# Kernel tuning notes

Measured on AMD Instinct MI355X. Metric: run time of the kernel, lower is better.

## Reference

```python
import jax, jax.numpy as jnp
import numpy as np

N_SPACE = 197  # spatial tokens (ViT-B/16: 196 patches + CLS)
T = 8          # frames, fixed by space_time_pos shape (197*8, dim)
H = 12         # heads


def setup_inputs() -> dict:
    key = jax.random.key(0)
    ks = jax.random.split(key, 8)
    dim = 768
    B = 8
    Nq = 1576
    scale = dim ** -0.5
    return {
        "s_x": jax.random.normal(ks[0], (N_SPACE, B * T, dim), jnp.float32),
        "t_x": jax.random.normal(ks[1], (B, Nq, dim), jnp.float32),
        "space_time_pos": scale * jax.random.normal(ks[2], (N_SPACE * T, dim), jnp.float32),
        "q_w": jax.random.normal(ks[3], (dim, dim), jnp.float32) * 0.02,
        "q_b": jnp.zeros((dim,), jnp.float32),
        "kv_w": jax.random.normal(ks[4], (2 * dim, dim), jnp.float32) * 0.02,
        "kv_b": jnp.zeros((2 * dim,), jnp.float32),
        "proj_w": jax.random.normal(ks[5], (dim, dim), jnp.float32) * 0.02,
        "proj_b": jnp.zeros((dim,), jnp.float32),
    }


def reference(s_x, t_x, space_time_pos, q_w, q_b, kv_w, kv_b, proj_w, proj_b):
    n, BT, dim = s_x.shape
    B, Nq, _ = t_x.shape
    t = BT // B
    head_dim = dim // H
    scale = head_dim ** -0.5

    # rearrange 'n (b t) d -> b (t n) d'
    s = s_x.reshape(n, B, t, dim).transpose(1, 2, 0, 3).reshape(B, t * n, dim)
    s = s + space_time_pos  # (B, t*n, dim)

    # Q from t_x, K/V from s
    q = t_x @ q_w.T + q_b                      # (B, Nq, dim)
    kv = s @ kv_w.T + kv_b                     # (B, t*n, 2*dim)
    Nk = t * n
    # 'b n (e h d) -> e b h n d'
    kv = kv.reshape(B, Nk, 2, H, head_dim).transpose(2, 0, 3, 1, 4)
    k, v = kv[0], kv[1]                        # (B, H, Nk, hd)
    q = q.reshape(B, Nq, H, head_dim).transpose(0, 2, 1, 3) * scale  # (B, H, Nq, hd)

    attn = jnp.einsum('bhqd,bhkd->bhqk', q, k)
    attn = jax.nn.softmax(attn, axis=-1)
    out = jnp.einsum('bhqk,bhkd->bhqd', attn, v)   # (B, H, Nq, hd)
    out = out.transpose(0, 2, 1, 3).reshape(B, Nq, dim)
    return out @ proj_w.T + proj_b
```

## Files before the change

kernel.cpp:

```cpp
#include <hip/hip_runtime.h>
#include <stdint.h>

#define NSPACE 197
#define TFRAMES 8
#define NH 12
#define DIM 768
#define HD 64
#define BATCH 8
#define NQ 1576
#define NK 1576
#define M_REAL 12608
#define M_PAD 12672
#define VT_LD 1600

typedef __attribute__((ext_vector_type(8))) short s16x8;
typedef __attribute__((ext_vector_type(4))) short s16x4;
typedef __attribute__((ext_vector_type(4))) float f32x4;

__device__ inline uint16_t f2bf(float f) {
    union { float f; uint32_t i; } c; c.f = f;
    uint32_t r = c.i + 0x7FFF + ((c.i >> 16) & 1);
    return (uint16_t)(r >> 16);
}

__device__ inline uint32_t cvtpk_bf16(float lo, float hi) {
    uint32_t r;
    asm("v_cvt_pk_bf16_f32 %0, %1, %2" : "=v"(r) : "v"(lo), "v"(hi));
    return r;
}

__device__ inline float exp2_raw(float x) { return __builtin_amdgcn_exp2f(x); }

__device__ inline void gld_lds16(const uint16_t* g, uint16_t* l) {
    __builtin_amdgcn_global_load_lds(
        (const __attribute__((address_space(1))) void*)g,
        (__attribute__((address_space(3))) void*)l,
        16, 0, 0);
}


__global__ void conv_f2b(const float* __restrict__ src, uint16_t* __restrict__ dst, int n8) {
    int chunk = blockIdx.x * 256 + threadIdx.x;
    if (chunk >= n8) return;
    size_t off = (size_t)chunk * 8;
    float4 a = *(const float4*)(src + off);
    float4 b = *(const float4*)(src + off + 4);
    union { s16x8 v; uint32_t u[4]; } o;
    o.u[0] = cvtpk_bf16(a.x, a.y);
    o.u[1] = cvtpk_bf16(a.z, a.w);
    o.u[2] = cvtpk_bf16(b.x, b.y);
    o.u[3] = cvtpk_bf16(b.z, b.w);
    *(s16x8*)(dst + off) = o.v;
}

__global__ void fill_x(const float* __restrict__ t_x, uint16_t* __restrict__ x_pad) {
    int chunk = blockIdx.x * 256 + threadIdx.x;
    const int total = M_PAD * (DIM / 8);
    if (chunk >= total) return;
    size_t off = (size_t)chunk * 8;
    s16x8 o;
    if (off < (size_t)M_REAL * DIM) {
        float4 a = *(const float4*)(t_x + off);
        float4 b = *(const float4*)(t_x + off + 4);
        union { s16x8 v; uint32_t u[4]; } p;
        p.u[0] = cvtpk_bf16(a.x, a.y);
        p.u[1] = cvtpk_bf16(a.z, a.w);
        p.u[2] = cvtpk_bf16(b.x, b.y);
        p.u[3] = cvtpk_bf16(b.z, b.w);
        o = p.v;
    } else {
        for (int j = 0; j < 8; j++) o[j] = 0;
    }
    *(s16x8*)(x_pad + off) = o;
}

__global__ void fill_s(const float* __restrict__ s_x, const float* __restrict__ pos,
                       uint16_t* __restrict__ s_pad) {
    int chunk = blockIdx.x * 256 + threadIdx.x;
    const int total = M_PAD * (DIM / 8);
    if (chunk >= total) return;
    int i = chunk / (DIM / 8);
    int cc = chunk - i * (DIM / 8);
    int d0 = cc * 8;
    uint16_t* dst = s_pad + (size_t)i * DIM + d0;
    if (i >= M_REAL) {
        s16x8 z; for (int j = 0; j < 8; j++) z[j] = 0;
        *(s16x8*)dst = z;
        return;
    }
    int b = i / NK, rr = i - b * NK;
    int t_i = rr / NSPACE, n_i = rr - t_i * NSPACE;
    const float* src = s_x + ((size_t)(n_i * (BATCH * TFRAMES) + b * TFRAMES + t_i)) * DIM + d0;
    const float* ps = pos + (size_t)rr * DIM + d0;
    float4 a0 = *(const float4*)src;
    float4 a1 = *(const float4*)(src + 4);
    float4 p0 = *(const float4*)ps;
    float4 p1 = *(const float4*)(ps + 4);
    union { s16x8 v; uint32_t u[4]; } o;
    o.u[0] = cvtpk_bf16(a0.x + p0.x, a0.y + p0.y);
    o.u[1] = cvtpk_bf16(a0.z + p0.z, a0.w + p0.w);
    o.u[2] = cvtpk_bf16(a1.x + p1.x, a1.y + p1.y);
    o.u[3] = cvtpk_bf16(a1.z + p1.z, a1.w + p1.w);
    *(s16x8*)dst = o.v;
}

template <int MODE>
__global__ __launch_bounds__(256)
void gemm_bt(const uint16_t* __restrict__ A, const uint16_t* __restrict__ W,
             const float* __restrict__ bias,
             uint16_t* __restrict__ out0, uint16_t* __restrict__ out1,
             float* __restrict__ outf) {
    __shared__ uint16_t As[2][128 * 32];
    __shared__ uint16_t Bs[2][128 * 32];
    const int t = threadIdx.x;
    const int lane = t & 63, w = t >> 6;
    const int r16 = lane & 15, quad = lane >> 4;
    const int wm = w >> 1, wn = w & 1;
    const int m0 = blockIdx.y * 128;
    const int n0 = blockIdx.x * 128;

    const int srow = w * 32 + (lane >> 2);
    const int scol = (lane & 3) * 8;
    const uint16_t* Ag = A + (size_t)(m0 + srow) * DIM + scol;
    const uint16_t* Wg = W + (size_t)(n0 + srow) * DIM + scol;
    const int lbase = w * 32 * 32;

    f32x4 acc[4][4];
    for (int a = 0; a < 4; a++)
        for (int bb = 0; bb < 4; bb++)
            for (int r = 0; r < 4; r++) acc[a][bb][r] = 0.f;

    auto stage = [&](int kkoff, int buf) {
        gld_lds16(Ag + kkoff, &As[buf][lbase]);
        gld_lds16(Ag + kkoff + (size_t)16 * DIM, &As[buf][lbase + 16 * 32]);
        gld_lds16(Wg + kkoff, &Bs[buf][lbase]);
        gld_lds16(Wg + kkoff + (size_t)16 * DIM, &Bs[buf][lbase + 16 * 32]);
    };
    auto compute = [&](int buf) {
        s16x8 af[4], bfr[4];
        #pragma unroll
        for (int mt = 0; mt < 4; mt++)
            af[mt] = *(const s16x8*)&As[buf][(wm * 64 + mt * 16 + r16) * 32 + quad * 8];
        #pragma unroll
        for (int nt = 0; nt < 4; nt++)
            bfr[nt] = *(const s16x8*)&Bs[buf][(wn * 64 + nt * 16 + r16) * 32 + quad * 8];
        #pragma unroll
        for (int mt = 0; mt < 4; mt++)
            #pragma unroll
            for (int nt = 0; nt < 4; nt++)
                acc[mt][nt] = __builtin_amdgcn_mfma_f32_16x16x32_bf16(af[mt], bfr[nt], acc[mt][nt], 0, 0, 0);
    };

    stage(0, 0);
    __syncthreads();

    for (int kk = 0; kk < DIM; kk += 64) {
        stage(kk + 32, 1);
        compute(0);
        __syncthreads();
        if (kk + 64 < DIM) stage(kk + 64, 0);
        compute(1);
        __syncthreads();
    }

    for (int mt = 0; mt < 4; mt++)
        for (int nt = 0; nt < 4; nt++) {
            int col = n0 + wn * 64 + nt * 16 + r16;
            float bz = bias[col];
            int rowb = m0 + wm * 64 + mt * 16 + quad * 4;
            for (int r = 0; r < 4; r++) {
                int i = rowb + r;
                if (i >= M_REAL) continue;
                float v = acc[mt][nt][r] + bz;
                if (MODE == 0) {
                    int b = i / NQ, nq = i - b * NQ;
                    int h = col >> 6, d = col & 63;
                    out0[(size_t)(((b * NH + h) * NQ) + nq) * HD + d] = f2bf(v * 0.18033688011112042f);
                } else if (MODE == 1) {
                    int b = i / NK, nk = i - b * NK;
                    if (col < DIM) {
                        int h = col >> 6, d = col & 63;
                        out0[(size_t)(((b * NH + h) * NK) + nk) * HD + d] = f2bf(v);
                    } else {
                        int c2 = col - DIM;
                        int h = c2 >> 6, d = c2 & 63;
                        out1[(size_t)(((b * NH + h) * NK) + nk) * HD + d] = f2bf(v);
                    }
                } else {
                    outf[(size_t)i * DIM + col] = v;
                }
            }
        }
}

__global__ __launch_bounds__(256)
void transpose_v(const uint16_t* __restrict__ v, uint16_t* __restrict__ vt) {
    __shared__ uint16_t T[64 * 72];
    int tile = blockIdx.x, bh = blockIdx.y;
    int nk0 = tile * 64;
    const uint16_t* V = v + (size_t)bh * NK * HD;
    uint16_t* VT = vt + (size_t)bh * HD * VT_LD;
    int tid = threadIdx.x;
    int rr = tid >> 3;
    int c8 = (tid & 7) * 8;
    for (int p = 0; p < 2; p++) {
        int lr = p * 32 + rr;
        int nk = nk0 + lr;
        s16x8 val;
        if (nk < NK) val = *(const s16x8*)(V + (size_t)nk * HD + c8);
        else for (int j = 0; j < 8; j++) val[j] = 0;
        for (int j = 0; j < 8; j++)
            T[(c8 + j) * 72 + lr] = (uint16_t)val[j];
    }
    __syncthreads();
    for (int p = 0; p < 2; p++) {
        int d = p * 32 + rr;
        s16x8 o = *(const s16x8*)&T[d * 72 + c8];
        *(s16x8*)(VT + (size_t)d * VT_LD + nk0 + c8) = o;
    }
}

#define NITER 50
__global__ __launch_bounds__(256)
void flash_attn(const uint16_t* __restrict__ q_buf, const uint16_t* __restrict__ k_buf,
                const uint16_t* __restrict__ vt_buf, uint16_t* __restrict__ ao) {
    __shared__ uint16_t Kb[2][32 * 72];
    __shared__ uint16_t Vb[2][64 * 40];
    int h = blockIdx.y, b = blockIdx.z;
    int tid = threadIdx.x;
    int lane = tid & 63, w = tid >> 6;
    int r16 = lane & 15, quad = lane >> 4;
    size_t bh = (size_t)(b * NH + h);
    const uint16_t* Q = q_buf + bh * NQ * HD;
    const uint16_t* K = k_buf + bh * NK * HD;
    const uint16_t* VT = vt_buf + bh * HD * VT_LD;
    int q0 = blockIdx.x * 128 + w * 32;

    const int kg = tid >> 3;
    const int kc = (tid & 7) * 8;
    const int kslot = ((kg >> 3) << 2) + (kg & 3) + ((kg & 4) ? 16 : 0);
    const int vd = tid >> 2;
    const int vc = (tid & 3) * 8;
    const uint16_t* Kg = K + (size_t)kg * HD + kc;
    const uint16_t* Vg = VT + (size_t)vd * VT_LD + vc;
    uint16_t* Kw = &Kb[0][kslot * 72 + kc];
    uint16_t* Vw = &Vb[0][vd * 40 + vc];
    const int KBSZ = 32 * 72, VBSZ = 64 * 40;

    s16x8 qf[2][2];
    for (int m = 0; m < 2; m++) {
        int qrow = q0 + m * 16 + r16;
        if (qrow < NQ) {
            qf[m][0] = *(const s16x8*)(Q + (size_t)qrow * HD + quad * 8);
            qf[m][1] = *(const s16x8*)(Q + (size_t)qrow * HD + 32 + quad * 8);
        } else {
            for (int j = 0; j < 8; j++) { qf[m][0][j] = 0; qf[m][1][j] = 0; }
        }
    }

    f32x4 z4;
    for (int r = 0; r < 4; r++) z4[r] = 0.f;

    f32x4 oT[2][4];
    f32x4 lsum4[2];
    for (int m = 0; m < 2; m++) {
        for (int dt = 0; dt < 4; dt++)
            for (int r = 0; r < 4; r++) oT[m][dt][r] = 0.f;
        for (int r = 0; r < 4; r++) lsum4[m][r] = 0.f;
    }

    {
        s16x8 kv = *(const s16x8*)Kg;
        s16x8 vv = *(const s16x8*)Vg;
        *(s16x8*)Kw = kv;
        *(s16x8*)Vw = vv;
    }
    __syncthreads();

    for (int it = 0; it < NITER - 1; it++) {
        int kb = it * 32;
        int cur = it & 1, nxt = cur ^ 1;
        s16x8 knv = *(const s16x8*)(Kg + (size_t)(kb + 32) * HD);
        s16x8 vnv = *(const s16x8*)(Vg + kb + 32);

        const uint16_t* Kc = &Kb[cur][0];
        const uint16_t* Vc = &Vb[cur][0];
        s16x8 kfA0 = *(const s16x8*)(Kc + r16 * 72 + quad * 8);
        s16x8 kfA1 = *(const s16x8*)(Kc + r16 * 72 + 32 + quad * 8);
        s16x8 kfB0 = *(const s16x8*)(Kc + (16 + r16) * 72 + quad * 8);
        s16x8 kfB1 = *(const s16x8*)(Kc + (16 + r16) * 72 + 32 + quad * 8);

        s16x8 pf[2];
        #pragma unroll
        for (int m = 0; m < 2; m++) {
            f32x4 sA = __builtin_amdgcn_mfma_f32_16x16x32_bf16(kfA0, qf[m][0], z4, 0, 0, 0);
            sA = __builtin_amdgcn_mfma_f32_16x16x32_bf16(kfA1, qf[m][1], sA, 0, 0, 0);
            f32x4 sB = __builtin_amdgcn_mfma_f32_16x16x32_bf16(kfB0, qf[m][0], z4, 0, 0, 0);
            sB = __builtin_amdgcn_mfma_f32_16x16x32_bf16(kfB1, qf[m][1], sB, 0, 0, 0);
            f32x4 pA, pB;
            #pragma unroll
            for (int r = 0; r < 4; r++) { pA[r] = exp2_raw(sA[r]); pB[r] = exp2_raw(sB[r]); }
            lsum4[m] += pA;
            lsum4[m] += pB;
            union { s16x8 v; uint32_t u[4]; } pk;
            pk.u[0] = cvtpk_bf16(pA[0], pA[1]);
            pk.u[1] = cvtpk_bf16(pA[2], pA[3]);
            pk.u[2] = cvtpk_bf16(pB[0], pB[1]);
            pk.u[3] = cvtpk_bf16(pB[2], pB[3]);
            pf[m] = pk.v;
        }
        #pragma unroll
        for (int dt = 0; dt < 4; dt++) {
            s16x8 vf = *(const s16x8*)(Vc + (dt * 16 + r16) * 40 + quad * 8);
            oT[0][dt] = __builtin_amdgcn_mfma_f32_16x16x32_bf16(vf, pf[0], oT[0][dt], 0, 0, 0);
            oT[1][dt] = __builtin_amdgcn_mfma_f32_16x16x32_bf16(vf, pf[1], oT[1][dt], 0, 0, 0);
        }
        *(s16x8*)(Kw + nxt * KBSZ) = knv;
        *(s16x8*)(Vw + nxt * VBSZ) = vnv;
        __syncthreads();
    }

    {
        const int it = NITER - 1;
        const int kb = it * 32;
        const int cur = it & 1;
        const uint16_t* Kc = &Kb[cur][0];
        const uint16_t* Vc = &Vb[cur][0];
        s16x8 kfA0 = *(const s16x8*)(Kc + r16 * 72 + quad * 8);
        s16x8 kfA1 = *(const s16x8*)(Kc + r16 * 72 + 32 + quad * 8);
        s16x8 kfB0 = *(const s16x8*)(Kc + (16 + r16) * 72 + quad * 8);
        s16x8 kfB1 = *(const s16x8*)(Kc + (16 + r16) * 72 + 32 + quad * 8);

        s16x8 pf[2];
        #pragma unroll
        for (int m = 0; m < 2; m++) {
            f32x4 sA = __builtin_amdgcn_mfma_f32_16x16x32_bf16(kfA0, qf[m][0], z4, 0, 0, 0);
            sA = __builtin_amdgcn_mfma_f32_16x16x32_bf16(kfA1, qf[m][1], sA, 0, 0, 0);
            f32x4 sB = __builtin_amdgcn_mfma_f32_16x16x32_bf16(kfB0, qf[m][0], z4, 0, 0, 0);
            sB = __builtin_amdgcn_mfma_f32_16x16x32_bf16(kfB1, qf[m][1], sB, 0, 0, 0);
            f32x4 pA, pB;
            #pragma unroll
            for (int r = 0; r < 4; r++) {
                pA[r] = (kb + quad * 8 + r < NK)     ? exp2_raw(sA[r]) : 0.f;
                pB[r] = (kb + quad * 8 + 4 + r < NK) ? exp2_raw(sB[r]) : 0.f;
            }
            lsum4[m] += pA;
            lsum4[m] += pB;
            union { s16x8 v; uint32_t u[4]; } pk;
            pk.u[0] = cvtpk_bf16(pA[0], pA[1]);
            pk.u[1] = cvtpk_bf16(pA[2], pA[3]);
            pk.u[2] = cvtpk_bf16(pB[0], pB[1]);
            pk.u[3] = cvtpk_bf16(pB[2], pB[3]);
            pf[m] = pk.v;
        }
        #pragma unroll
        for (int dt = 0; dt < 4; dt++) {
            s16x8 vf = *(const s16x8*)(Vc + (dt * 16 + r16) * 40 + quad * 8);
            oT[0][dt] = __builtin_amdgcn_mfma_f32_16x16x32_bf16(vf, pf[0], oT[0][dt], 0, 0, 0);
            oT[1][dt] = __builtin_amdgcn_mfma_f32_16x16x32_bf16(vf, pf[1], oT[1][dt], 0, 0, 0);
        }
    }

    #pragma unroll
    for (int m = 0; m < 2; m++) {
        float rs = lsum4[m][0] + lsum4[m][1] + lsum4[m][2] + lsum4[m][3];
        rs += __shfl_xor(rs, 16);
        rs += __shfl_xor(rs, 32);
        int q = q0 + m * 16 + r16;
        if (q >= NQ) continue;
        float inv = 1.0f / rs;
        size_t rowoff = (size_t)(b * NQ + q) * DIM + h * HD;
        #pragma unroll
        for (int dt = 0; dt < 4; dt++) {
            union { s16x4 v; uint32_t u[2]; } o;
            o.u[0] = cvtpk_bf16(oT[m][dt][0] * inv, oT[m][dt][1] * inv);
            o.u[1] = cvtpk_bf16(oT[m][dt][2] * inv, oT[m][dt][3] * inv);
            *(s16x4*)(ao + rowoff + dt * 16 + quad * 4) = o.v;
        }
    }
}

extern "C" void kernel_launch(void* const* d_in, const int* in_sizes, int n_in,
                              void* d_out, int out_size, void* d_ws, size_t ws_size,
                              hipStream_t stream) {
    const float* s_x    = (const float*)d_in[0];
    const float* t_x    = (const float*)d_in[1];
    const float* pos    = (const float*)d_in[2];
    const float* q_w    = (const float*)d_in[3];
    const float* q_b    = (const float*)d_in[4];
    const float* kv_w   = (const float*)d_in[5];
    const float* kv_b   = (const float*)d_in[6];
    const float* proj_w = (const float*)d_in[7];
    const float* proj_b = (const float*)d_in[8];
    float* out = (float*)d_out;

    char* ws = (char*)d_ws;
    size_t off = 0;
    auto carve = [&](size_t bytes) {
        void* p = ws + off;
        off += (bytes + 255) & ~(size_t)255;
        return p;
    };
    uint16_t* x_pad  = (uint16_t*)carve((size_t)M_PAD * DIM * 2);
    uint16_t* s_pad  = (uint16_t*)carve((size_t)M_PAD * DIM * 2);
    uint16_t* q_buf  = (uint16_t*)carve((size_t)BATCH * NH * NQ * HD * 2);
    uint16_t* k_buf  = (uint16_t*)carve((size_t)BATCH * NH * NK * HD * 2);
    uint16_t* vt_buf = (uint16_t*)carve((size_t)BATCH * NH * HD * VT_LD * 2);
    uint16_t* wbuf   = (uint16_t*)carve((size_t)2 * DIM * DIM * 2);
    if (off > ws_size) return;
    uint16_t* v_buf = x_pad;
    uint16_t* ao    = x_pad;

    const int fill_blocks = (M_PAD * (DIM / 8) + 255) / 256;
    const int wq8 = DIM * DIM / 8, wkv8 = 2 * DIM * DIM / 8;

    fill_x<<<fill_blocks, 256, 0, stream>>>(t_x, x_pad);
    fill_s<<<fill_blocks, 256, 0, stream>>>(s_x, pos, s_pad);

    conv_f2b<<<(wq8 + 255) / 256, 256, 0, stream>>>(q_w, wbuf, wq8);
    gemm_bt<0><<<dim3(DIM / 128, M_PAD / 128), 256, 0, stream>>>(x_pad, wbuf, q_b, q_buf, nullptr, nullptr);

    conv_f2b<<<(wkv8 + 255) / 256, 256, 0, stream>>>(kv_w, wbuf, wkv8);
    gemm_bt<1><<<dim3(2 * DIM / 128, M_PAD / 128), 256, 0, stream>>>(s_pad, wbuf, kv_b, k_buf, v_buf, nullptr);
    transpose_v<<<dim3(VT_LD / 64, BATCH * NH), 256, 0, stream>>>(v_buf, vt_buf);

    flash_attn<<<dim3((NQ + 127) / 128, NH, BATCH), 256, 0, stream>>>(q_buf, k_buf, vt_buf, ao);

    conv_f2b<<<(wq8 + 255) / 256, 256, 0, stream>>>(proj_w, wbuf, wq8);
    gemm_bt<2><<<dim3(DIM / 128, M_PAD / 128), 256, 0, stream>>>(ao, wbuf, proj_b, nullptr, nullptr, out);
}
```

Measured before the change: 367.9 us.

## Fuse Q and KV projections into one GEMM launch and write V transposed directly

Merges the Q projection and KV projection GEMMs into a single launch whose grid covers 18 column blocks, choosing input, weight and bias per block. The V half of the epilogue now writes four consecutive rows as one packed store straight into the transposed V layout, so the separate transpose_v kernel and its intermediate buffer traffic go away. A small kernel zeroes the padded tail of the transposed buffer, and the Q and KV weights get separate buffers so both conversions can run ahead of the fused GEMM. This aims to cut launch count, improve GPU fill, and remove a full read and write of V. The cost is more branching in the epilogue.

```diff
diff --git a/kernel.cpp b/kernel.cpp
--- a/kernel.cpp
+++ b/kernel.cpp
@@ -104,12 +104,116 @@
     *(s16x8*)dst = o.v;
 }
 
-template <int MODE>
+__global__ void zero_vt_tail(uint16_t* __restrict__ vt) {
+    int bh = blockIdx.x;
+    int tid = threadIdx.x;
+    int d = tid >> 2;
+    int j = tid & 3;
+    uint32_t* p = (uint32_t*)(vt + (size_t)bh * HD * VT_LD + (size_t)d * VT_LD + NK + j * 6);
+    p[0] = 0; p[1] = 0; p[2] = 0;
+}
+
 __global__ __launch_bounds__(256)
-void gemm_bt(const uint16_t* __restrict__ A, const uint16_t* __restrict__ W,
-             const float* __restrict__ bias,
-             uint16_t* __restrict__ out0, uint16_t* __restrict__ out1,
-             float* __restrict__ outf) {
+void gemm_qkv(const uint16_t* __restrict__ x_pad, const uint16_t* __restrict__ s_pad,
+              const uint16_t* __restrict__ wq, const uint16_t* __restrict__ wkv,
+              const float* __restrict__ q_bias, const float* __restrict__ kv_bias,
+              uint16_t* __restrict__ q_buf, uint16_t* __restrict__ k_buf,
+              uint16_t* __restrict__ vt_buf) {
+    __shared__ uint16_t As[2][128 * 32];
+    __shared__ uint16_t Bs[2][128 * 32];
+    const int t = threadIdx.x;
+    const int lane = t & 63, w = t >> 6;
+    const int r16 = lane & 15, quad = lane >> 4;
+    const int wm = w >> 1, wn = w & 1;
+    const int m0 = blockIdx.y * 128;
+    const bool isQ = blockIdx.x < 6;
+    const int n0 = (isQ ? blockIdx.x : blockIdx.x - 6) * 128;
+    const uint16_t* A = isQ ? x_pad : s_pad;
+    const uint16_t* W = isQ ? wq : wkv;
+    const float* bias = isQ ? q_bias : kv_bias;
+
+    const int srow = w * 32 + (lane >> 2);
+    const int scol = (lane & 3) * 8;
+    const uint16_t* Ag = A + (size_t)(m0 + srow) * DIM + scol;
+    const uint16_t* Wg = W + (size_t)(n0 + srow) * DIM + scol;
+    const int lbase = w * 32 * 32;
+
+    f32x4 acc[4][4];
+    for (int a = 0; a < 4; a++)
+        for (int bb = 0; bb < 4; bb++)
+            for (int r = 0; r < 4; r++) acc[a][bb][r] = 0.f;
+
+    auto stage = [&](int kkoff, int buf) {
+        gld_lds16(Ag + kkoff, &As[buf][lbase]);
+        gld_lds16(Ag + kkoff + (size_t)16 * DIM, &As[buf][lbase + 16 * 32]);
+        gld_lds16(Wg + kkoff, &Bs[buf][lbase]);
+        gld_lds16(Wg + kkoff + (size_t)16 * DIM, &Bs[buf][lbase + 16 * 32]);
+    };
+    auto compute = [&](int buf) {
+        s16x8 af[4], bfr[4];
+        #pragma unroll
+        for (int mt = 0; mt < 4; mt++)
+            af[mt] = *(const s16x8*)&As[buf][(wm * 64 + mt * 16 + r16) * 32 + quad * 8];
+        #pragma unroll
+        for (int nt = 0; nt < 4; nt++)
+            bfr[nt] = *(const s16x8*)&Bs[buf][(wn * 64 + nt * 16 + r16) * 32 + quad * 8];
+        #pragma unroll
+        for (int mt = 0; mt < 4; mt++)
+            #pragma unroll
+            for (int nt = 0; nt < 4; nt++)
+                acc[mt][nt] = __builtin_amdgcn_mfma_f32_16x16x32_bf16(af[mt], bfr[nt], acc[mt][nt], 0, 0, 0);
+    };
+
+    stage(0, 0);
+    __syncthreads();
+    for (int kk = 0; kk < DIM; kk += 64) {
+        stage(kk + 32, 1);
+        compute(0);
+        __syncthreads();
+        if (kk + 64 < DIM) stage(kk + 64, 0);
+        compute(1);
+        __syncthreads();
+    }
+
+    for (int mt = 0; mt < 4; mt++)
+        for (int nt = 0; nt < 4; nt++) {
+            int col = n0 + wn * 64 + nt * 16 + r16;
+            float bz = bias[col];
+            int rowb = m0 + wm * 64 + mt * 16 + quad * 4;
+            if (rowb >= M_REAL) continue;
+            if (isQ) {
+                for (int r = 0; r < 4; r++) {
+                    int i = rowb + r;
+                    float v = acc[mt][nt][r] + bz;
+                    int b = i / NQ, nq = i - b * NQ;
+                    int h = col >> 6, d = col & 63;
+                    q_buf[(size_t)(((b * NH + h) * NQ) + nq) * HD + d] = f2bf(v * 0.18033688011112042f);
+                }
+            } else if (col < DIM) {
+                for (int r = 0; r < 4; r++) {
+                    int i = rowb + r;
+                    float v = acc[mt][nt][r] + bz;
+                    int b = i / NK, nk = i - b * NK;
+                    int h = col >> 6, d = col & 63;
+                    k_buf[(size_t)(((b * NH + h) * NK) + nk) * HD + d] = f2bf(v);
+                }
+            } else {
+                int c2 = col - DIM;
+                int h = c2 >> 6, d = c2 & 63;
+                int b = rowb / NK, nk = rowb - b * NK;
+                s16x4 o;
+                o[0] = (short)f2bf(acc[mt][nt][0] + bz);
+                o[1] = (short)f2bf(acc[mt][nt][1] + bz);
+                o[2] = (short)f2bf(acc[mt][nt][2] + bz);
+                o[3] = (short)f2bf(acc[mt][nt][3] + bz);
+                *(s16x4*)(vt_buf + ((size_t)(b * NH + h) * HD + d) * VT_LD + nk) = o;
+            }
+        }
+}
+
+__global__ __launch_bounds__(256)
+void gemm_proj(const uint16_t* __restrict__ A, const uint16_t* __restrict__ W,
+               const float* __restrict__ bias, float* __restrict__ outf) {
     __shared__ uint16_t As[2][128 * 32];
     __shared__ uint16_t Bs[2][128 * 32];
     const int t = threadIdx.x;
@@ -153,7 +257,6 @@
 
     stage(0, 0);
     __syncthreads();
-
     for (int kk = 0; kk < DIM; kk += 64) {
         stage(kk + 32, 1);
         compute(0);
@@ -171,53 +274,9 @@
             for (int r = 0; r < 4; r++) {
                 int i = rowb + r;
                 if (i >= M_REAL) continue;
-                float v = acc[mt][nt][r] + bz;
-                if (MODE == 0) {
-                    int b = i / NQ, nq = i - b * NQ;
-                    int h = col >> 6, d = col & 63;
-                    out0[(size_t)(((b * NH + h) * NQ) + nq) * HD + d] = f2bf(v * 0.18033688011112042f);
-                } else if (MODE == 1) {
-                    int b = i / NK, nk = i - b * NK;
-                    if (col < DIM) {
-                        int h = col >> 6, d = col & 63;
-                        out0[(size_t)(((b * NH + h) * NK) + nk) * HD + d] = f2bf(v);
-                    } else {
-                        int c2 = col - DIM;
-                        int h = c2 >> 6, d = c2 & 63;
-                        out1[(size_t)(((b * NH + h) * NK) + nk) * HD + d] = f2bf(v);
-                    }
-                } else {
-                    outf[(size_t)i * DIM + col] = v;
-                }
+                outf[(size_t)i * DIM + col] = acc[mt][nt][r] + bz;
             }
         }
-}
-
-__global__ __launch_bounds__(256)
-void transpose_v(const uint16_t* __restrict__ v, uint16_t* __restrict__ vt) {
-    __shared__ uint16_t T[64 * 72];
-    int tile = blockIdx.x, bh = blockIdx.y;
-    int nk0 = tile * 64;
-    const uint16_t* V = v + (size_t)bh * NK * HD;
-    uint16_t* VT = vt + (size_t)bh * HD * VT_LD;
-    int tid = threadIdx.x;
-    int rr = tid >> 3;
-    int c8 = (tid & 7) * 8;
-    for (int p = 0; p < 2; p++) {
-        int lr = p * 32 + rr;
-        int nk = nk0 + lr;
-        s16x8 val;
-        if (nk < NK) val = *(const s16x8*)(V + (size_t)nk * HD + c8);
-        else for (int j = 0; j < 8; j++) val[j] = 0;
-        for (int j = 0; j < 8; j++)
-            T[(c8 + j) * 72 + lr] = (uint16_t)val[j];
-    }
-    __syncthreads();
-    for (int p = 0; p < 2; p++) {
-        int d = p * 32 + rr;
-        s16x8 o = *(const s16x8*)&T[d * 72 + c8];
-        *(s16x8*)(VT + (size_t)d * VT_LD + nk0 + c8) = o;
-    }
 }
 
 #define NITER 50
@@ -401,31 +460,30 @@
         off += (bytes + 255) & ~(size_t)255;
         return p;
     };
-    uint16_t* x_pad  = (uint16_t*)carve((size_t)M_PAD * DIM * 2);
-    uint16_t* s_pad  = (uint16_t*)carve((size_t)M_PAD * DIM * 2);
-    uint16_t* q_buf  = (uint16_t*)carve((size_t)BATCH * NH * NQ * HD * 2);
-    uint16_t* k_buf  = (uint16_t*)carve((size_t)BATCH * NH * NK * HD * 2);
-    uint16_t* vt_buf = (uint16_t*)carve((size_t)BATCH * NH * HD * VT_LD * 2);
-    uint16_t* wbuf   = (uint16_t*)carve((size_t)2 * DIM * DIM * 2);
+    uint16_t* x_pad   = (uint16_t*)carve((size_t)M_PAD * DIM * 2);
+    uint16_t* s_pad   = (uint16_t*)carve((size_t)M_PAD * DIM * 2);
+    uint16_t* q_buf   = (uint16_t*)carve((size_t)BATCH * NH * NQ * HD * 2);
+    uint16_t* k_buf   = (uint16_t*)carve((size_t)BATCH * NH * NK * HD * 2);
+    uint16_t* vt_buf  = (uint16_t*)carve((size_t)BATCH * NH * HD * VT_LD * 2);
+    uint16_t* wq_buf  = (uint16_t*)carve((size_t)DIM * DIM * 2);
+    uint16_t* wkv_buf = (uint16_t*)carve((size_t)2 * DIM * DIM * 2);
     if (off > ws_size) return;
-    uint16_t* v_buf = x_pad;
-    uint16_t* ao    = x_pad;
+    uint16_t* ao = x_pad;
 
     const int fill_blocks = (M_PAD * (DIM / 8) + 255) / 256;
     const int wq8 = DIM * DIM / 8, wkv8 = 2 * DIM * DIM / 8;
 
     fill_x<<<fill_blocks, 256, 0, stream>>>(t_x, x_pad);
     fill_s<<<fill_blocks, 256, 0, stream>>>(s_x, pos, s_pad);
-
-    conv_f2b<<<(wq8 + 255) / 256, 256, 0, stream>>>(q_w, wbuf, wq8);
-    gemm_bt<0><<<dim3(DIM / 128, M_PAD / 128), 256, 0, stream>>>(x_pad, wbuf, q_b, q_buf, nullptr, nullptr);
-
-    conv_f2b<<<(wkv8 + 255) / 256, 256, 0, stream>>>(kv_w, wbuf, wkv8);
-    gemm_bt<1><<<dim3(2 * DIM / 128, M_PAD / 128), 256, 0, stream>>>(s_pad, wbuf, kv_b, k_buf, v_buf, nullptr);
-    transpose_v<<<dim3(VT_LD / 64, BATCH * NH), 256, 0, stream>>>(v_buf, vt_buf);
+    conv_f2b<<<(wq8 + 255) / 256, 256, 0, stream>>>(q_w, wq_buf, wq8);
+    conv_f2b<<<(wkv8 + 255) / 256, 256, 0, stream>>>(kv_w, wkv_buf, wkv8);
+    zero_vt_tail<<<BATCH * NH, 256, 0, stream>>>(vt_buf);
+
+    gemm_qkv<<<dim3(18, M_PAD / 128), 256, 0, stream>>>(
+        x_pad, s_pad, wq_buf, wkv_buf, q_b, kv_b, q_buf, k_buf, vt_buf);
 
     flash_attn<<<dim3((NQ + 127) / 128, NH, BATCH), 256, 0, stream>>>(q_buf, k_buf, vt_buf, ao);
 
-    conv_f2b<<<(wq8 + 255) / 256, 256, 0, stream>>>(proj_w, wbuf, wq8);
-    gemm_bt<2><<<dim3(DIM / 128, M_PAD / 128), 256, 0, stream>>>(ao, wbuf, proj_b, nullptr, nullptr, out);
-}
+    conv_f2b<<<(wq8 + 255) / 256, 256, 0, stream>>>(proj_w, wq_buf, wq8);
+    gemm_proj<<<dim3(DIM / 128, M_PAD / 128), 256, 0, stream>>>(ao, wq_buf, proj_b, out);
+}
```

After: 803.6 us. +118.4%, slower.
